# Kernel tuning notes

Measured on AMD Instinct MI355X. Metric: run time of the kernel, lower is better.

The kernel has to match this reference:

```python
import jax, jax.numpy as jnp
import numpy as np

N_HEAD, D_MODEL, D_HEAD = 16, 1024, 64
LN_EPS = 1e-5
SCALE = 1.0 / (D_HEAD ** 0.5)


def _rel_shift(x):
    # x: [qlen, klen, bsz, n_head]
    q, k, b, n = x.shape
    zero_pad = jnp.zeros((q, 1, b, n), x.dtype)
    x_padded = jnp.concatenate([zero_pad, x], axis=1)        # [q, k+1, b, n]
    x_padded = x_padded.reshape(k + 1, q, b, n)
    return x_padded[1:].reshape(q, k, b, n)


def setup_inputs() -> dict:
    key = jax.random.key(0)
    ks = jax.random.split(key, 8)
    qlen, bsz = 2048, 4
    H = N_HEAD * D_HEAD
    s = 0.02
    return {
        "w": jax.random.normal(ks[0], (qlen, bsz, D_MODEL), jnp.float32),
        "r": jax.random.normal(ks[1], (qlen, D_MODEL), jnp.float32),
        "qkv_w": jax.random.normal(ks[2], (3 * H, D_MODEL), jnp.float32) * s,
        "r_net_w": jax.random.normal(ks[3], (H, D_MODEL), jnp.float32) * s,
        "o_w": jax.random.normal(ks[4], (D_MODEL, H), jnp.float32) * s,
        "r_w_bias": jax.random.normal(ks[5], (N_HEAD, D_HEAD), jnp.float32) * s,
        "r_r_bias": jax.random.normal(ks[6], (N_HEAD, D_HEAD), jnp.float32) * s,
        "ln_g": jnp.ones((D_MODEL,), jnp.float32),
        "ln_b": jnp.zeros((D_MODEL,), jnp.float32),
    }


def _layer_norm(x, g, b):
    mu = jnp.mean(x, axis=-1, keepdims=True)
    var = jnp.var(x, axis=-1, keepdims=True)
    return (x - mu) * jax.lax.rsqrt(var + LN_EPS) * g + b


def reference(w, r, qkv_w, r_net_w, o_w, r_w_bias, r_r_bias, ln_g, ln_b):
    qlen, bsz, _ = w.shape
    rlen = r.shape[0]
    H = N_HEAD * D_HEAD

    w_heads = jnp.einsum('ibm,hm->ibh', w, qkv_w)            # [q,b,3H]
    r_head_k = jnp.einsum('jm,hm->jh', r, r_net_w)           # [r,H]

    w_head_q = w_heads[..., :H].reshape(qlen, bsz, N_HEAD, D_HEAD)
    w_head_k = w_heads[..., H:2 * H].reshape(qlen, bsz, N_HEAD, D_HEAD)
    w_head_v = w_heads[..., 2 * H:].reshape(qlen, bsz, N_HEAD, D_HEAD)
    r_head_k = r_head_k.reshape(rlen, N_HEAD, D_HEAD)

    AC = jnp.einsum('ibnd,jbnd->ijbn', w_head_q + r_w_bias, w_head_k)
    BD = jnp.einsum('ibnd,jnd->ijbn', w_head_q + r_r_bias, r_head_k)
    BD = _rel_shift(BD)

    attn_score = (AC + BD) * SCALE                           # [q,k,b,n]
    attn_prob = jax.nn.softmax(attn_score, axis=1)

    attn_vec = jnp.einsum('ijbn,jbnd->ibnd', attn_prob, w_head_v)
    attn_vec = attn_vec.reshape(qlen, bsz, H)
    attn_out = jnp.einsum('ibh,mh->ibm', attn_vec, o_w)

    return _layer_norm(w + attn_out, ln_g, ln_b)
```

## Files before the change

### kernel.cpp

```cpp
#include <hip/hip_runtime.h>
#include <hip/hip_bf16.h>
#include <stdint.h>

using bf16 = __hip_bfloat16;
typedef __attribute__((ext_vector_type(8))) short bf16x8;
typedef __attribute__((ext_vector_type(4))) float f32x4;

#define SCALE 0.125f

__device__ __forceinline__ float b2f(bf16 x) { return __bfloat162float(x); }
__device__ __forceinline__ bf16 f2b(float x) { return __float2bfloat16(x); }

__global__ __launch_bounds__(256) void cvt_kernel(const float* __restrict__ in, bf16* __restrict__ out, int n4) {
  int i = blockIdx.x * 256 + threadIdx.x;
  if (i >= n4) return;
  float4 v = ((const float4*)in)[i];
  alignas(8) bf16 o[4];
  o[0] = f2b(v.x); o[1] = f2b(v.y); o[2] = f2b(v.z); o[3] = f2b(v.w);
  ((uint2*)out)[i] = *(const uint2*)o;
}

template<int STORE_BF16>
__global__ __launch_bounds__(256) void gemm_bt(const bf16* __restrict__ A, const bf16* __restrict__ B,
                                               void* __restrict__ C, int M, int N, int K) {
  __shared__ bf16 As[128][72];
  __shared__ bf16 Bs[128][72];
  const int tid = threadIdx.x;
  const int lane = tid & 63;
  const int w = tid >> 6, wr = w >> 1, wc = w & 1;
  const int m0 = blockIdx.y * 128, n0 = blockIdx.x * 128;
  const int lr = lane & 15, lg = lane >> 4;
  f32x4 acc[4][4] = {};
  for (int k0 = 0; k0 < K; k0 += 64) {
    __syncthreads();
#pragma unroll
    for (int i = 0; i < 4; ++i) {
      int c = tid + i * 256;
      int row = c >> 3, seg = c & 7;
      *(int4*)&As[row][seg * 8] = *(const int4*)&A[(size_t)(m0 + row) * K + k0 + seg * 8];
      *(int4*)&Bs[row][seg * 8] = *(const int4*)&B[(size_t)(n0 + row) * K + k0 + seg * 8];
    }
    __syncthreads();
#pragma unroll
    for (int kk = 0; kk < 2; ++kk) {
      bf16x8 af[4], bfv[4];
#pragma unroll
      for (int m = 0; m < 4; ++m) af[m] = *(const bf16x8*)&As[wr * 64 + m * 16 + lr][kk * 32 + lg * 8];
#pragma unroll
      for (int n = 0; n < 4; ++n) bfv[n] = *(const bf16x8*)&Bs[wc * 64 + n * 16 + lr][kk * 32 + lg * 8];
#pragma unroll
      for (int m = 0; m < 4; ++m)
#pragma unroll
        for (int n = 0; n < 4; ++n)
          acc[m][n] = __builtin_amdgcn_mfma_f32_16x16x32_bf16(af[m], bfv[n], acc[m][n], 0, 0, 0);
    }
  }
#pragma unroll
  for (int m = 0; m < 4; ++m)
#pragma unroll
    for (int n = 0; n < 4; ++n)
#pragma unroll
      for (int r = 0; r < 4; ++r) {
        int row = m0 + wr * 64 + m * 16 + lg * 4 + r;
        int col = n0 + wc * 64 + n * 16 + lr;
        if (STORE_BF16) ((bf16*)C)[(size_t)row * N + col] = f2b(acc[m][n][r]);
        else            ((float*)C)[(size_t)row * N + col] = acc[m][n][r];
      }
}

__global__ __launch_bounds__(256) void flash_kernel(const bf16* __restrict__ wh, const bf16* __restrict__ rk,
                                                    const float* __restrict__ rwb, const float* __restrict__ rrb,
                                                    bf16* __restrict__ av) {
  const int bn = blockIdx.y;
  const int b = bn >> 4, n = bn & 15;
  const int q0 = blockIdx.x * 64;
  const int tid = threadIdx.x, lane = tid & 63, w = tid >> 6;
  const int lr = lane & 15, lg = lane >> 4;
  __shared__ bf16 Ks[64][72];
  __shared__ bf16 Vt[64][72];
  __shared__ bf16 Ps[64][72];
  __shared__ bf16 Tp[64][128];

  bf16x8 qf[2], qrf[2][2];
#pragma unroll
  for (int kk = 0; kk < 2; ++kk) {
    {
      int row = q0 + w * 16 + lr;
      int4 raw = *(const int4*)&wh[((size_t)row * 4 + b) * 3072 + n * 64 + kk * 32 + lg * 8];
      const bf16* rp = (const bf16*)&raw;
      alignas(16) bf16 ov[8];
#pragma unroll
      for (int e = 0; e < 8; ++e) ov[e] = f2b((b2f(rp[e]) + rwb[n * 64 + kk * 32 + lg * 8 + e]) * SCALE);
      qf[kk] = *(const bf16x8*)ov;
    }
#pragma unroll
    for (int ao = 0; ao < 2; ++ao) {
      int row = q0 + ao + w * 16 + lr; if (row > 2047) row = 2047;
      int4 raw = *(const int4*)&wh[((size_t)row * 4 + b) * 3072 + n * 64 + kk * 32 + lg * 8];
      const bf16* rp = (const bf16*)&raw;
      alignas(16) bf16 ov[8];
#pragma unroll
      for (int e = 0; e < 8; ++e) ov[e] = f2b((b2f(rp[e]) + rrb[n * 64 + kk * 32 + lg * 8 + e]) * SCALE);
      qrf[ao][kk] = *(const bf16x8*)ov;
    }
  }

  auto panel = [&](int pbase, int sub) {
    const int aidx = sub ? 1 : 0;
#pragma unroll
    for (int nt = 0; nt < 4; ++nt) {
      int c = pbase + nt * 16 + lr - sub;
      c = c < 0 ? 0 : (c > 2047 ? 2047 : c);
      f32x4 pacc = {};
#pragma unroll
      for (int kk = 0; kk < 2; ++kk) {
        bf16x8 bfrag = *(const bf16x8*)&rk[(size_t)c * 1024 + n * 64 + kk * 32 + lg * 8];
        pacc = __builtin_amdgcn_mfma_f32_16x16x32_bf16(qrf[aidx][kk], bfrag, pacc, 0, 0, 0);
      }
      int cm = (pbase + nt * 16 + lr) & 127;
#pragma unroll
      for (int r = 0; r < 4; ++r) Tp[w * 16 + lg * 4 + r][cm] = f2b(pacc[r]);
    }
  };

  panel(1984 - q0, 0);

  float mrow[4] = {-1e30f, -1e30f, -1e30f, -1e30f};
  float lrow[4] = {0.f, 0.f, 0.f, 0.f};
  f32x4 oacc[4] = {};

  for (int j0 = 0; j0 < 2048; j0 += 64) {
    const int t = j0 - q0;
    __syncthreads();
#pragma unroll
    for (int i = 0; i < 2; ++i) {
      int c = tid + i * 256;
      int row = c >> 3, seg = c & 7;
      *(int4*)&Ks[row][seg * 8] = *(const int4*)&wh[((size_t)(j0 + row) * 4 + b) * 3072 + 1024 + n * 64 + seg * 8];
      int4 vv = *(const int4*)&wh[((size_t)(j0 + row) * 4 + b) * 3072 + 2048 + n * 64 + seg * 8];
      const bf16* vp = (const bf16*)&vv;
#pragma unroll
      for (int e = 0; e < 8; ++e) Vt[seg * 8 + e][row] = vp[e];
    }
    __syncthreads();

    if (t <= -64) panel(t + 2048, 0);
    else          panel(t, 2);

    f32x4 s[4] = {};
#pragma unroll
    for (int kk = 0; kk < 2; ++kk)
#pragma unroll
      for (int f = 0; f < 4; ++f) {
        bf16x8 kf = *(const bf16x8*)&Ks[f * 16 + lr][kk * 32 + lg * 8];
        s[f] = __builtin_amdgcn_mfma_f32_16x16x32_bf16(qf[kk], kf, s[f], 0, 0, 0);
      }
#pragma unroll
    for (int f = 0; f < 4; ++f)
#pragma unroll
      for (int r = 0; r < 4; ++r) {
        int i = q0 + w * 16 + lg * 4 + r;
        int j = j0 + f * 16 + lr;
        int u = j - i;
        float bd = 0.f;
        if (u != 1) {
          int cm = (u >= 2 ? u : u + 2047) & 127;
          bd = b2f(Tp[w * 16 + lg * 4 + r][cm]);
        }
        s[f][r] += bd;
      }
    float al[4];
#pragma unroll
    for (int r = 0; r < 4; ++r) {
      float mx = fmaxf(fmaxf(s[0][r], s[1][r]), fmaxf(s[2][r], s[3][r]));
#pragma unroll
      for (int msk = 1; msk <= 8; msk <<= 1) mx = fmaxf(mx, __shfl_xor(mx, msk));
      float mnew = fmaxf(mrow[r], mx);
      al[r] = __expf(mrow[r] - mnew);
      float rs = 0.f;
#pragma unroll
      for (int f = 0; f < 4; ++f) { float p = __expf(s[f][r] - mnew); s[f][r] = p; rs += p; }
#pragma unroll
      for (int msk = 1; msk <= 8; msk <<= 1) rs += __shfl_xor(rs, msk);
      lrow[r] = lrow[r] * al[r] + rs;
      mrow[r] = mnew;
    }
#pragma unroll
    for (int f = 0; f < 4; ++f)
#pragma unroll
      for (int r = 0; r < 4; ++r) Ps[w * 16 + lg * 4 + r][f * 16 + lr] = f2b(s[f][r]);
#pragma unroll
    for (int df = 0; df < 4; ++df) {
      oacc[df][0] *= al[0]; oacc[df][1] *= al[1]; oacc[df][2] *= al[2]; oacc[df][3] *= al[3];
    }
#pragma unroll
    for (int kk = 0; kk < 2; ++kk) {
      bf16x8 pf = *(const bf16x8*)&Ps[w * 16 + lr][kk * 32 + lg * 8];
#pragma unroll
      for (int df = 0; df < 4; ++df) {
        bf16x8 vf = *(const bf16x8*)&Vt[df * 16 + lr][kk * 32 + lg * 8];
        oacc[df] = __builtin_amdgcn_mfma_f32_16x16x32_bf16(pf, vf, oacc[df], 0, 0, 0);
      }
    }
  }
#pragma unroll
  for (int df = 0; df < 4; ++df)
#pragma unroll
    for (int r = 0; r < 4; ++r) {
      int i = q0 + w * 16 + lg * 4 + r;
      av[((size_t)i * 4 + b) * 1024 + n * 64 + df * 16 + lr] = f2b(oacc[df][r] / lrow[r]);
    }
}

__global__ __launch_bounds__(256) void ln_kernel(const float* __restrict__ w, const float* __restrict__ ao,
                                                 const float* __restrict__ g, const float* __restrict__ bb,
                                                 float* __restrict__ out) {
  const int row = blockIdx.x;
  const int t = threadIdx.x;
  const float4 wv = ((const float4*)(w + (size_t)row * 1024))[t];
  const float4 av = ((const float4*)(ao + (size_t)row * 1024))[t];
  float x0 = wv.x + av.x, x1 = wv.y + av.y, x2 = wv.z + av.z, x3 = wv.w + av.w;
  float s1 = x0 + x1 + x2 + x3;
  float s2 = x0 * x0 + x1 * x1 + x2 * x2 + x3 * x3;
#pragma unroll
  for (int m = 1; m <= 32; m <<= 1) { s1 += __shfl_xor(s1, m); s2 += __shfl_xor(s2, m); }
  __shared__ float red[8];
  const int lane = t & 63, wv2 = t >> 6;
  if (lane == 0) { red[wv2] = s1; red[4 + wv2] = s2; }
  __syncthreads();
  s1 = red[0] + red[1] + red[2] + red[3];
  s2 = red[4] + red[5] + red[6] + red[7];
  const float mu = s1 * (1.f / 1024.f);
  const float var = s2 * (1.f / 1024.f) - mu * mu;
  const float rr = rsqrtf(var + 1e-5f);
  const float4 gv = ((const float4*)g)[t];
  const float4 bv = ((const float4*)bb)[t];
  float4 o;
  o.x = (x0 - mu) * rr * gv.x + bv.x;
  o.y = (x1 - mu) * rr * gv.y + bv.y;
  o.z = (x2 - mu) * rr * gv.z + bv.z;
  o.w = (x3 - mu) * rr * gv.w + bv.w;
  ((float4*)(out + (size_t)row * 1024))[t] = o;
}

extern "C" void kernel_launch(void* const* d_in, const int* in_sizes, int n_in,
                              void* d_out, int out_size, void* d_ws, size_t ws_size,
                              hipStream_t stream) {
  const float* w    = (const float*)d_in[0];
  const float* r    = (const float*)d_in[1];
  const float* qkvw = (const float*)d_in[2];
  const float* rnw  = (const float*)d_in[3];
  const float* ow   = (const float*)d_in[4];
  const float* rwb  = (const float*)d_in[5];
  const float* rrb  = (const float*)d_in[6];
  const float* lng  = (const float*)d_in[7];
  const float* lnb  = (const float*)d_in[8];
  float* out = (float*)d_out;

  char* ws = (char*)d_ws;
  size_t off = 0;
  auto alloc = [&](size_t bytes) -> char* {
    char* p = ws + off; off += (bytes + 255) & ~((size_t)255); return p;
  };
  bf16*  wb  = (bf16*)alloc((size_t)8192 * 1024 * 2);
  bf16*  qb  = (bf16*)alloc((size_t)3072 * 1024 * 2);
  bf16*  rb  = (bf16*)alloc((size_t)2048 * 1024 * 2);
  bf16*  rnb = (bf16*)alloc((size_t)1024 * 1024 * 2);
  bf16*  owb = (bf16*)alloc((size_t)1024 * 1024 * 2);
  bf16*  wh  = (bf16*)alloc((size_t)8192 * 3072 * 2);
  bf16*  rkb = (bf16*)alloc((size_t)2048 * 1024 * 2);
  bf16*  avb = (bf16*)alloc((size_t)8192 * 1024 * 2);
  float* ao  = (float*)alloc((size_t)8192 * 1024 * 4);

  auto cvt = [&](const float* in, bf16* o, size_t nelem) {
    int n4 = (int)(nelem / 4);
    cvt_kernel<<<dim3((n4 + 255) / 256), dim3(256), 0, stream>>>(in, o, n4);
  };
  cvt(w, wb, (size_t)8192 * 1024);
  cvt(qkvw, qb, (size_t)3072 * 1024);
  cvt(r, rb, (size_t)2048 * 1024);
  cvt(rnw, rnb, (size_t)1024 * 1024);
  cvt(ow, owb, (size_t)1024 * 1024);

  gemm_bt<1><<<dim3(3072 / 128, 8192 / 128), dim3(256), 0, stream>>>(wb, qb, wh, 8192, 3072, 1024);
  gemm_bt<1><<<dim3(1024 / 128, 2048 / 128), dim3(256), 0, stream>>>(rb, rnb, rkb, 2048, 1024, 1024);

  flash_kernel<<<dim3(32, 64), dim3(256), 0, stream>>>(wh, rkb, rwb, rrb, avb);

  gemm_bt<0><<<dim3(1024 / 128, 8192 / 128), dim3(256), 0, stream>>>(avb, owb, ao, 8192, 1024, 1024);
  ln_kernel<<<dim3(8192), dim3(256), 0, stream>>>(w, ao, lng, lnb, out);
}
```

Baseline: 686.9 us.

## Prefetch K/V and rel-pos tiles into registers and XOR-swizzle LDS tiles

Restructures the flash attention loop so the next K/V tile is loaded into registers during the current tile's compute. The relative-position key rows for two tiles ahead are also prefetched, and the BD panel for the next tile is computed at the end of each iteration. Padded LDS arrays are replaced by XOR-swizzled layouts to avoid bank conflicts without extra space, and launch bounds request 4 blocks per CU. This aims to hide global load latency behind MFMA work, at the cost of more live registers, which may limit occupancy.

```diff
diff --git a/kernel.cpp b/kernel.cpp
--- a/kernel.cpp
+++ b/kernel.cpp
@@ -68,17 +68,17 @@
       }
 }
 
-__global__ __launch_bounds__(256) void flash_kernel(const bf16* __restrict__ wh, const bf16* __restrict__ rk,
-                                                    const float* __restrict__ rwb, const float* __restrict__ rrb,
-                                                    bf16* __restrict__ av) {
+__global__ __launch_bounds__(256, 4) void flash_kernel(const bf16* __restrict__ wh, const bf16* __restrict__ rk,
+                                                       const float* __restrict__ rwb, const float* __restrict__ rrb,
+                                                       bf16* __restrict__ av) {
   const int bn = blockIdx.y;
   const int b = bn >> 4, n = bn & 15;
   const int q0 = blockIdx.x * 64;
   const int tid = threadIdx.x, lane = tid & 63, w = tid >> 6;
   const int lr = lane & 15, lg = lane >> 4;
-  __shared__ bf16 Ks[64][72];
-  __shared__ bf16 Vt[64][72];
-  __shared__ bf16 Ps[64][72];
+  __shared__ bf16 Ks[64][64];
+  __shared__ bf16 Vt[64][64];
+  __shared__ bf16 Ps[64][64];
   __shared__ bf16 Tp[64][128];
 
   bf16x8 qf[2], qrf[2][2];
@@ -105,70 +105,109 @@
     }
   }
 
-  auto panel = [&](int pbase, int sub) {
+  auto coords = [&](int u, int& pbase, int& sub) {
+    int tt = 64 * u - q0;
+    if (tt <= -64) { pbase = tt + 2048; sub = 0; } else { pbase = tt; sub = 2; }
+  };
+  auto rk_row = [&](int pbase, int sub, int nt) {
+    int c = pbase + nt * 16 + lr - sub;
+    return c < 0 ? 0 : (c > 2047 ? 2047 : c);
+  };
+
+  auto panel_f = [&](int pbase, int sub, const bf16x8* bfr) {
     const int aidx = sub ? 1 : 0;
 #pragma unroll
     for (int nt = 0; nt < 4; ++nt) {
-      int c = pbase + nt * 16 + lr - sub;
-      c = c < 0 ? 0 : (c > 2047 ? 2047 : c);
       f32x4 pacc = {};
-#pragma unroll
-      for (int kk = 0; kk < 2; ++kk) {
-        bf16x8 bfrag = *(const bf16x8*)&rk[(size_t)c * 1024 + n * 64 + kk * 32 + lg * 8];
-        pacc = __builtin_amdgcn_mfma_f32_16x16x32_bf16(qrf[aidx][kk], bfrag, pacc, 0, 0, 0);
-      }
+      pacc = __builtin_amdgcn_mfma_f32_16x16x32_bf16(qrf[aidx][0], bfr[nt * 2 + 0], pacc, 0, 0, 0);
+      pacc = __builtin_amdgcn_mfma_f32_16x16x32_bf16(qrf[aidx][1], bfr[nt * 2 + 1], pacc, 0, 0, 0);
       int cm = (pbase + nt * 16 + lr) & 127;
 #pragma unroll
       for (int r = 0; r < 4; ++r) Tp[w * 16 + lg * 4 + r][cm] = f2b(pacc[r]);
     }
   };
-
-  panel(1984 - q0, 0);
+  auto panel_direct = [&](int pbase, int sub) {
+    bf16x8 bfr[8];
+#pragma unroll
+    for (int nt = 0; nt < 4; ++nt) {
+      int c = rk_row(pbase, sub, nt);
+      bfr[nt * 2 + 0] = *(const bf16x8*)&rk[(size_t)c * 1024 + n * 64 + lg * 8];
+      bfr[nt * 2 + 1] = *(const bf16x8*)&rk[(size_t)c * 1024 + n * 64 + 32 + lg * 8];
+    }
+    panel_f(pbase, sub, bfr);
+  };
+
+  panel_direct(1984 - q0, 0);
+  { int pb, sb; coords(0, pb, sb); panel_direct(pb, sb); }
+
+  int4 kreg[2], vreg[2];
+  bf16x8 rkf[8];
+  auto kv_prefetch = [&](int j0) {
+#pragma unroll
+    for (int i = 0; i < 2; ++i) {
+      int c = tid + i * 256;
+      int row = c >> 3, seg = c & 7;
+      kreg[i] = *(const int4*)&wh[((size_t)(j0 + row) * 4 + b) * 3072 + 1024 + n * 64 + seg * 8];
+      vreg[i] = *(const int4*)&wh[((size_t)(j0 + row) * 4 + b) * 3072 + 2048 + n * 64 + seg * 8];
+    }
+  };
+  auto rk_prefetch = [&](int u) {
+    int pb, sb; coords(u, pb, sb);
+#pragma unroll
+    for (int nt = 0; nt < 4; ++nt) {
+      int c = rk_row(pb, sb, nt);
+      rkf[nt * 2 + 0] = *(const bf16x8*)&rk[(size_t)c * 1024 + n * 64 + lg * 8];
+      rkf[nt * 2 + 1] = *(const bf16x8*)&rk[(size_t)c * 1024 + n * 64 + 32 + lg * 8];
+    }
+  };
+
+  kv_prefetch(0);
+  rk_prefetch(1);
 
   float mrow[4] = {-1e30f, -1e30f, -1e30f, -1e30f};
   float lrow[4] = {0.f, 0.f, 0.f, 0.f};
   f32x4 oacc[4] = {};
 
-  for (int j0 = 0; j0 < 2048; j0 += 64) {
-    const int t = j0 - q0;
+  for (int u = 0; u < 32; ++u) {
+    const int j0 = u * 64;
     __syncthreads();
 #pragma unroll
     for (int i = 0; i < 2; ++i) {
       int c = tid + i * 256;
       int row = c >> 3, seg = c & 7;
-      *(int4*)&Ks[row][seg * 8] = *(const int4*)&wh[((size_t)(j0 + row) * 4 + b) * 3072 + 1024 + n * 64 + seg * 8];
-      int4 vv = *(const int4*)&wh[((size_t)(j0 + row) * 4 + b) * 3072 + 2048 + n * 64 + seg * 8];
-      const bf16* vp = (const bf16*)&vv;
-#pragma unroll
-      for (int e = 0; e < 8; ++e) Vt[seg * 8 + e][row] = vp[e];
-    }
+      *(int4*)&Ks[row][(seg ^ (row & 7)) * 8] = kreg[i];
+      const bf16* vp = (const bf16*)&vreg[i];
+#pragma unroll
+      for (int e = 0; e < 8; ++e) {
+        int d = seg * 8 + e;
+        Vt[d][row ^ (((e ^ seg) & 7) << 3)] = vp[e];
+      }
+    }
+    if (u < 31) kv_prefetch(j0 + 64);
     __syncthreads();
 
-    if (t <= -64) panel(t + 2048, 0);
-    else          panel(t, 2);
-
     f32x4 s[4] = {};
 #pragma unroll
     for (int kk = 0; kk < 2; ++kk)
 #pragma unroll
       for (int f = 0; f < 4; ++f) {
-        bf16x8 kf = *(const bf16x8*)&Ks[f * 16 + lr][kk * 32 + lg * 8];
+        int row = f * 16 + lr;
+        bf16x8 kf = *(const bf16x8*)&Ks[row][((kk * 4 + lg) ^ (row & 7)) * 8];
         s[f] = __builtin_amdgcn_mfma_f32_16x16x32_bf16(qf[kk], kf, s[f], 0, 0, 0);
       }
 #pragma unroll
-    for (int f = 0; f < 4; ++f)
+    for (int f = 0; f < 4; ++f) {
+      int jj = j0 + f * 16 + lr;
 #pragma unroll
       for (int r = 0; r < 4; ++r) {
         int i = q0 + w * 16 + lg * 4 + r;
-        int j = j0 + f * 16 + lr;
-        int u = j - i;
-        float bd = 0.f;
-        if (u != 1) {
-          int cm = (u >= 2 ? u : u + 2047) & 127;
-          bd = b2f(Tp[w * 16 + lg * 4 + r][cm]);
+        int uu = jj - i;
+        if (uu != 1) {
+          int cm = (uu >= 2 ? uu : uu - 1) & 127;
+          s[f][r] += b2f(Tp[w * 16 + lg * 4 + r][cm]);
         }
-        s[f][r] += bd;
-      }
+      }
+    }
     float al[4];
 #pragma unroll
     for (int r = 0; r < 4; ++r) {
@@ -188,19 +227,29 @@
 #pragma unroll
     for (int f = 0; f < 4; ++f)
 #pragma unroll
-      for (int r = 0; r < 4; ++r) Ps[w * 16 + lg * 4 + r][f * 16 + lr] = f2b(s[f][r]);
+      for (int r = 0; r < 4; ++r) {
+        int row = w * 16 + lg * 4 + r;
+        Ps[row][(f * 16 + lr) ^ ((row & 7) << 3)] = f2b(s[f][r]);
+      }
 #pragma unroll
     for (int df = 0; df < 4; ++df) {
       oacc[df][0] *= al[0]; oacc[df][1] *= al[1]; oacc[df][2] *= al[2]; oacc[df][3] *= al[3];
     }
 #pragma unroll
     for (int kk = 0; kk < 2; ++kk) {
-      bf16x8 pf = *(const bf16x8*)&Ps[w * 16 + lr][kk * 32 + lg * 8];
+      bf16x8 pf = *(const bf16x8*)&Ps[w * 16 + lr][((kk * 4 + lg) ^ (lr & 7)) * 8];
 #pragma unroll
       for (int df = 0; df < 4; ++df) {
-        bf16x8 vf = *(const bf16x8*)&Vt[df * 16 + lr][kk * 32 + lg * 8];
+        int d = df * 16 + lr;
+        int vz = (d & 7) ^ ((d >> 3) & 7);
+        bf16x8 vf = *(const bf16x8*)&Vt[d][((kk * 4 + lg) ^ vz) * 8];
         oacc[df] = __builtin_amdgcn_mfma_f32_16x16x32_bf16(pf, vf, oacc[df], 0, 0, 0);
       }
+    }
+    if (u < 31) {
+      int pb, sb; coords(u + 1, pb, sb);
+      panel_f(pb, sb, rkf);
+      if (u < 30) rk_prefetch(u + 2);
     }
   }
 #pragma unroll
```

After: 1.713 ms. +149.4%, slower.
